# Kernel optimization log

Hardware: AMD Instinct MI355X
Metric: run time of the kernel (lower is better)

The kernel has to match this reference:

```python
import jax, jax.numpy as jnp
import numpy as np

DIM = 2048
NUM_HEADS = 16
HEAD_DIM = DIM // NUM_HEADS  # 128
B, L = 2, 2048


def setup_inputs() -> dict:
    key = jax.random.key(0)
    ks = jax.random.split(key, 5)
    x = jax.random.normal(ks[0], (B, L, DIM), dtype=jnp.float32)
    # genuine RoPE tables: inv_freq over half the head dim
    half = HEAD_DIM // 2
    inv_freq = 1.0 / (10000.0 ** (jnp.arange(half, dtype=jnp.float32) / half))
    ang = jnp.arange(L, dtype=jnp.float32)[:, None] * inv_freq[None, :]  # (L, half)
    cos = jnp.cos(ang)[:, None, :]  # (L, 1, half) broadcasts over (B,L,H,half)
    sin = jnp.sin(ang)[:, None, :]
    def dw_init(k, shape):
        fan_in, fan_out = shape
        std = 1.0 / np.sqrt(fan_in) * min(1.0, np.sqrt(fan_out / fan_in))
        return jax.random.normal(k, shape, dtype=jnp.float32) * std
    Wq = dw_init(ks[1], (DIM, DIM))
    Wk = dw_init(ks[2], (DIM, HEAD_DIM))
    Wv = dw_init(ks[3], (DIM, HEAD_DIM))
    Wo = dw_init(ks[4], (DIM, DIM))  # random instead of zeros so output is nontrivial
    return {"x": x, "cos": cos, "sin": sin, "Wq": Wq, "Wk": Wk, "Wv": Wv, "Wo": Wo}


def apply_rotary_emb(x, cos, sin):
    x1, x2 = jnp.split(x, 2, axis=-1)
    return jnp.concatenate([x1 * cos + x2 * sin, x1 * -sin + x2 * cos], axis=-1)


def rms_norm(x):
    return x * jax.lax.rsqrt(jnp.mean(x * x, axis=-1, keepdims=True) + 1e-6)


def reference(x, cos, sin, Wq, Wk, Wv, Wo):
    Bb, Ll, _ = x.shape
    q = (x @ Wq).reshape(Bb, Ll, NUM_HEADS, HEAD_DIM)  # (B,L,H,D)
    k = (x @ Wk)  # (B,L,D)  single KV head (MQA)
    v = (x @ Wv)  # (B,L,D)
    q = rms_norm(apply_rotary_emb(q, cos, sin))
    k = rms_norm(apply_rotary_emb(k[:, :, None, :], cos, sin))[:, :, 0, :]  # (B,L,D)
    scale = 1.0 / jnp.sqrt(jnp.asarray(HEAD_DIM, dtype=x.dtype))
    # scores without materializing broadcasted K: (B,H,Lq,Lk)
    scores = jnp.einsum('bqhd,bkd->bhqk', q, k) * scale
    causal = jnp.tril(jnp.ones((Ll, Ll), dtype=jnp.bool_))
    scores = jnp.where(causal[None, None], scores, jnp.asarray(-jnp.inf, dtype=scores.dtype))
    attn = jax.nn.softmax(scores, axis=-1)
    out = jnp.einsum('bhqk,bkd->bqhd', attn, v).reshape(Bb, Ll, DIM)
    return out @ Wo
```

## Files before the change

### kernel.cpp

```cpp
#include <hip/hip_runtime.h>

#define DIM 2048
#define NH 16
#define HD 128
#define BB 2
#define LL 2048
#define MROWS (BB * LL)
#define NKV 2304
#define NT 32

typedef __attribute__((ext_vector_type(8))) short short8;
typedef __attribute__((ext_vector_type(4))) float floatx4;

__device__ inline ushort f2bf(float f) {
    union { float f; unsigned u; } v; v.f = f;
    unsigned r = v.u + 0x7FFFu + ((v.u >> 16) & 1u);
    return (ushort)(r >> 16);
}

__device__ __forceinline__ ushort f2bf_fast(float f) {
    __bf16 h = (__bf16)f;
    return __builtin_bit_cast(unsigned short, h);
}

#define GL16(g, l)                                                         \
    __builtin_amdgcn_global_load_lds(                                      \
        (const __attribute__((address_space(1))) unsigned int*)(g),        \
        (__attribute__((address_space(3))) unsigned int*)(l), 16, 0, 0)

__device__ __forceinline__ short8 ld8(const ushort* p) {
    return *reinterpret_cast<const short8*>(p);
}

__global__ __launch_bounds__(256) void prep(const float* __restrict__ x,
                                            ushort* __restrict__ xb,
                                            const float* __restrict__ Wq,
                                            const float* __restrict__ Wk,
                                            const float* __restrict__ Wv,
                                            const float* __restrict__ Wo,
                                            ushort* __restrict__ Wcatt,
                                            ushort* __restrict__ Wot) {
    __shared__ ushort T[64][72];
    const int bid = blockIdx.x;
    const int tid = threadIdx.x;
    if (bid < 4096) {
        size_t i = ((size_t)bid * 256 + tid) * 8;
        float4 a = *reinterpret_cast<const float4*>(x + i);
        float4 b = *reinterpret_cast<const float4*>(x + i + 4);
        ushort o[8] = {f2bf(a.x), f2bf(a.y), f2bf(a.z), f2bf(a.w),
                       f2bf(b.x), f2bf(b.y), f2bf(b.z), f2bf(b.w)};
        *reinterpret_cast<uint4*>(xb + i) = *reinterpret_cast<uint4*>(o);
        return;
    }
    const int wb = bid - 4096;
    const float* in;
    ushort* out;
    int in_ld, c0, r0;
    const int out_ld = 2048;
    if (wb < 1024) {
        in = Wq; out = Wcatt; in_ld = 2048;
        c0 = (wb & 31) * 64; r0 = (wb >> 5) * 64;
    } else if (wb < 2048) {
        int t = wb - 1024;
        in = Wo; out = Wot; in_ld = 2048;
        c0 = (t & 31) * 64; r0 = (t >> 5) * 64;
    } else if (wb < 2112) {
        int t = wb - 2048;
        in = Wk; out = Wcatt + (size_t)2048 * 2048; in_ld = 128;
        c0 = (t & 1) * 64; r0 = (t >> 1) * 64;
    } else {
        int t = wb - 2112;
        in = Wv; out = Wcatt + (size_t)2176 * 2048; in_ld = 128;
        c0 = (t & 1) * 64; r0 = (t >> 1) * 64;
    }
#pragma unroll
    for (int rep = 0; rep < 4; ++rep) {
        int idx = tid + rep * 256;
        int r = idx >> 4, c4 = idx & 15;
        float4 f = *reinterpret_cast<const float4*>(
            in + (size_t)(r0 + r) * in_ld + c0 + c4 * 4);
        T[r][c4 * 4 + 0] = f2bf(f.x);
        T[r][c4 * 4 + 1] = f2bf(f.y);
        T[r][c4 * 4 + 2] = f2bf(f.z);
        T[r][c4 * 4 + 3] = f2bf(f.w);
    }
    __syncthreads();
#pragma unroll
    for (int rep = 0; rep < 4; ++rep) {
        int idx = tid + rep * 256;
        int cr = idx >> 4, rc4 = idx & 15;
        uint a0 = (uint)T[rc4 * 4 + 0][cr] | ((uint)T[rc4 * 4 + 1][cr] << 16);
        uint a1 = (uint)T[rc4 * 4 + 2][cr] | ((uint)T[rc4 * 4 + 3][cr] << 16);
        uint2 val = {a0, a1};
        *reinterpret_cast<uint2*>(
            out + (size_t)(c0 + cr) * out_ld + r0 + rc4 * 4) = val;
    }
}

template <int U>
__device__ __forceinline__ void stage_unit(const ushort* __restrict__ A,
                                           const ushort* __restrict__ Bt,
                                           ushort* lbase, uint offA, uint offB,
                                           int t) {
    if (t >= NT) return;
    const ushort* g = (U < 2) ? Bt : A;
    uint off = ((U < 2) ? offB : offA) + ((U & 1) ? 128u * 2048u : 0u) +
               (uint)t * 64u;
    ushort* l = lbase + U * 8192;
    GL16(g + off, l + (size_t)threadIdx.x * 8);
    GL16(g + off + 64u * 2048u, l + (size_t)(threadIdx.x + 512) * 8);
}

__global__ __launch_bounds__(512)
__attribute__((amdgpu_waves_per_eu(2, 2)))
void gemm2p(const ushort* __restrict__ A,
            const ushort* __restrict__ Bt,
            float* __restrict__ Y, int N) {
    __shared__ __attribute__((aligned(16))) ushort lds[65536];
    const int tid = threadIdx.x;
    const int lane = tid & 63;
    const int w = tid >> 6;
    const int wm = w >> 2, wn = w & 3;
    const int col = lane & 15, quad = lane >> 4;
    const int sel = col & 7;
    const int L = blockIdx.y * 9 + blockIdx.x;
    const int x8 = L & 7, jj = L >> 3;
    const int bx = jj % 9;
    const int by = x8 * 2 + jj / 9;
    const int m0 = by * 256, n0 = bx * 256;

    const int r0 = tid >> 3;
    const int gc0 = (tid & 7) ^ (r0 & 7);
    const uint offA = (uint)(m0 + r0) * 2048u + (uint)gc0 * 8u;
    const uint offB = (uint)(n0 + r0) * 2048u + (uint)gc0 * 8u;

    floatx4 acc[8][4];
#pragma unroll
    for (int mt = 0; mt < 8; ++mt)
#pragma unroll
        for (int nt = 0; nt < 4; ++nt) acc[mt][nt] = (floatx4){0.f, 0.f, 0.f, 0.f};

    const int aoff0 = (2 + wm) * 8192 + col * 64;
    const int boff0 = (wn >> 1) * 8192 + ((wn & 1) * 64 + col) * 64;
    const int koff0 = (quad ^ sel) * 8;
    const int koff1 = ((4 + quad) ^ sel) * 8;

    stage_unit<0>(A, Bt, lds, offA, offB, 0);
    stage_unit<1>(A, Bt, lds, offA, offB, 0);
    stage_unit<2>(A, Bt, lds, offA, offB, 0);
    stage_unit<3>(A, Bt, lds, offA, offB, 0);
    asm volatile("s_waitcnt vmcnt(0)" ::: "memory");
    __builtin_amdgcn_s_barrier();

#pragma unroll 2
    for (int t = 0; t < NT; ++t) {
        ushort* lb = lds + (t & 1) * 32768;
        ushort* lbn = lds + ((t + 1) & 1) * 32768;

        short8 a0[8], b0[4];
#pragma unroll
        for (int mt = 0; mt < 8; ++mt)
            a0[mt] = ld8(lb + aoff0 + mt * 1024 + koff0);
#pragma unroll
        for (int nt = 0; nt < 4; ++nt)
            b0[nt] = ld8(lb + boff0 + nt * 1024 + koff0);
        stage_unit<0>(A, Bt, lbn, offA, offB, t + 1);
        stage_unit<1>(A, Bt, lbn, offA, offB, t + 1);
        stage_unit<2>(A, Bt, lbn, offA, offB, t + 1);
        stage_unit<3>(A, Bt, lbn, offA, offB, t + 1);
        __builtin_amdgcn_s_setprio(1);
#pragma unroll
        for (int mt = 0; mt < 8; ++mt)
#pragma unroll
            for (int nt = 0; nt < 4; ++nt)
                acc[mt][nt] = __builtin_amdgcn_mfma_f32_16x16x32_bf16(
                    a0[mt], b0[nt], acc[mt][nt], 0, 0, 0);
        __builtin_amdgcn_s_setprio(0);

        short8 a1[8], b1[4];
#pragma unroll
        for (int mt = 0; mt < 8; ++mt)
            a1[mt] = ld8(lb + aoff0 + mt * 1024 + koff1);
#pragma unroll
        for (int nt = 0; nt < 4; ++nt)
            b1[nt] = ld8(lb + boff0 + nt * 1024 + koff1);
        __builtin_amdgcn_s_setprio(1);
#pragma unroll
        for (int mt = 0; mt < 8; ++mt)
#pragma unroll
            for (int nt = 0; nt < 4; ++nt)
                acc[mt][nt] = __builtin_amdgcn_mfma_f32_16x16x32_bf16(
                    a1[mt], b1[nt], acc[mt][nt], 0, 0, 0);
        __builtin_amdgcn_s_setprio(0);
        asm volatile("s_waitcnt vmcnt(0)" ::: "memory");
        __builtin_amdgcn_s_barrier();
    }

#pragma unroll
    for (int mt = 0; mt < 8; ++mt)
#pragma unroll
        for (int nt = 0; nt < 4; ++nt)
#pragma unroll
            for (int rr = 0; rr < 4; ++rr)
                Y[(size_t)(m0 + wm * 128 + mt * 16 + quad * 4 + rr) * N + n0 +
                  wn * 64 + nt * 16 + col] = acc[mt][nt][rr];
}

template <int U>
__device__ __forceinline__ void stage_po(const ushort* __restrict__ A,
                                         const ushort* __restrict__ Bt,
                                         ushort* lbase, uint offA, uint offB,
                                         int t) {
    if (t >= NT) return;
    const ushort* g = (U < 2) ? Bt : A;
    uint off = ((U < 2) ? offB : offA) + ((U == 1) ? 128u * 2048u : 0u) +
               (uint)t * 64u;
    ushort* l = lbase + U * 8192;
    GL16(g + off, l + (size_t)threadIdx.x * 8);
    GL16(g + off + 64u * 2048u, l + (size_t)(threadIdx.x + 512) * 8);
}

__global__ __launch_bounds__(512)
__attribute__((amdgpu_waves_per_eu(2, 2)))
void gemm2pw(const ushort* __restrict__ A,
             const ushort* __restrict__ Bt,
             float* __restrict__ Y, int N) {
    __shared__ __attribute__((aligned(16))) ushort lds[49152];
    const int tid = threadIdx.x;
    const int lane = tid & 63;
    const int w = tid >> 6;
    const int wm = w >> 2, wn = w & 3;
    const int col = lane & 15, quad = lane >> 4;
    const int sel = col & 7;
    const int L = blockIdx.y * 8 + blockIdx.x;
    const int x8 = L & 7, jj = L >> 3;
    const int bx = (x8 & 1) * 4 + (jj & 3);
    const int by = (x8 >> 1) * 8 + (jj >> 2);
    const int m0 = by * 128, n0 = bx * 256;

    const int r0 = tid >> 3;
    const int gc0 = (tid & 7) ^ (r0 & 7);
    const uint offA = (uint)(m0 + r0) * 2048u + (uint)gc0 * 8u;
    const uint offB = (uint)(n0 + r0) * 2048u + (uint)gc0 * 8u;

    floatx4 acc[4][4];
#pragma unroll
    for (int mt = 0; mt < 4; ++mt)
#pragma unroll
        for (int nt = 0; nt < 4; ++nt) acc[mt][nt] = (floatx4){0.f, 0.f, 0.f, 0.f};

    const int aoff0 = 16384 + wm * 4096 + col * 64;
    const int boff0 = (wn >> 1) * 8192 + ((wn & 1) * 64 + col) * 64;
    const int koff0 = (quad ^ sel) * 8;
    const int koff1 = ((4 + quad) ^ sel) * 8;

    stage_po<0>(A, Bt, lds, offA, offB, 0);
    stage_po<1>(A, Bt, lds, offA, offB, 0);
    stage_po<2>(A, Bt, lds, offA, offB, 0);
    asm volatile("s_waitcnt vmcnt(0)" ::: "memory");
    __builtin_amdgcn_s_barrier();

#pragma unroll 2
    for (int t = 0; t < NT; ++t) {
        ushort* lb = lds + (t & 1) * 24576;
        ushort* lbn = lds + ((t + 1) & 1) * 24576;

        short8 a0[4], b0[4];
#pragma unroll
        for (int mt = 0; mt < 4; ++mt)
            a0[mt] = ld8(lb + aoff0 + mt * 1024 + koff0);
#pragma unroll
        for (int nt = 0; nt < 4; ++nt)
            b0[nt] = ld8(lb + boff0 + nt * 1024 + koff0);
        stage_po<0>(A, Bt, lbn, offA, offB, t + 1);
        stage_po<1>(A, Bt, lbn, offA, offB, t + 1);
        stage_po<2>(A, Bt, lbn, offA, offB, t + 1);
        __builtin_amdgcn_s_setprio(1);
#pragma unroll
        for (int mt = 0; mt < 4; ++mt)
#pragma unroll
            for (int nt = 0; nt < 4; ++nt)
                acc[mt][nt] = __builtin_amdgcn_mfma_f32_16x16x32_bf16(
                    a0[mt], b0[nt], acc[mt][nt], 0, 0, 0);
        __builtin_amdgcn_s_setprio(0);

        short8 a1[4], b1[4];
#pragma unroll
        for (int mt = 0; mt < 4; ++mt)
            a1[mt] = ld8(lb + aoff0 + mt * 1024 + koff1);
#pragma unroll
        for (int nt = 0; nt < 4; ++nt)
            b1[nt] = ld8(lb + boff0 + nt * 1024 + koff1);
        __builtin_amdgcn_s_setprio(1);
#pragma unroll
        for (int mt = 0; mt < 4; ++mt)
#pragma unroll
            for (int nt = 0; nt < 4; ++nt)
                acc[mt][nt] = __builtin_amdgcn_mfma_f32_16x16x32_bf16(
                    a1[mt], b1[nt], acc[mt][nt], 0, 0, 0);
        __builtin_amdgcn_s_setprio(0);
        asm volatile("s_waitcnt vmcnt(0)" ::: "memory");
        __builtin_amdgcn_s_barrier();
    }

#pragma unroll
    for (int mt = 0; mt < 4; ++mt)
#pragma unroll
        for (int nt = 0; nt < 4; ++nt)
#pragma unroll
            for (int rr = 0; rr < 4; ++rr)
                Y[(size_t)(m0 + wm * 64 + mt * 16 + quad * 4 + rr) * N + n0 +
                  wn * 64 + nt * 16 + col] = acc[mt][nt][rr];
}

__device__ __forceinline__ void rope_row(const float* __restrict__ in,
                                         ushort* __restrict__ outb,
                                         const float* __restrict__ cosb,
                                         const float* __restrict__ sinb,
                                         int row, int heads, int in_ld,
                                         int lane) {
    int token = row / heads, head = row % heads;
    int l = token & (LL - 1);
    const float* p = in + (size_t)token * in_ld + head * HD;
    float x1 = p[lane];
    float x2 = p[lane + 64];
    float c = cosb[l * 64 + lane];
    float s = sinb[l * 64 + lane];
    float o1 = x1 * c + x2 * s;
    float o2 = -x1 * s + x2 * c;
    float ss = o1 * o1 + o2 * o2;
#pragma unroll
    for (int off = 32; off > 0; off >>= 1) ss += __shfl_xor(ss, off);
    float r = rsqrtf(ss * (1.0f / 128.0f) + 1e-6f);
    outb[(size_t)row * HD + lane] = f2bf(o1 * r);
    outb[(size_t)row * HD + lane + 64] = f2bf(o2 * r);
}

__global__ __launch_bounds__(256) void rope_vt(const float* __restrict__ qkv,
                                               ushort* __restrict__ qb,
                                               ushort* __restrict__ kb,
                                               ushort* __restrict__ vt,
                                               const float* __restrict__ cosb,
                                               const float* __restrict__ sinb) {
    __shared__ ushort T[64][72];
    const int bid = blockIdx.x;
    const int tid = threadIdx.x;
    const int lane = tid & 63;
    if (bid < 16384) {
        int row = bid * 4 + (tid >> 6);
        rope_row(qkv, qb, cosb, sinb, row, NH, NKV, lane);
        return;
    }
    if (bid < 17408) {
        int row = (bid - 16384) * 4 + (tid >> 6);
        rope_row(qkv + DIM, kb, cosb, sinb, row, 1, NKV, lane);
        return;
    }
    const int t = bid - 17408;
    const int l0 = (t & 31) * 64, d0 = ((t >> 5) & 1) * 64, b = t >> 6;
    const float* v = qkv + DIM + HD;
#pragma unroll
    for (int rep = 0; rep < 4; ++rep) {
        int idx = tid + rep * 256;
        int r = idx >> 4, c4 = idx & 15;
        float4 f = *reinterpret_cast<const float4*>(
            v + (size_t)(b * LL + l0 + r) * NKV + d0 + c4 * 4);
        T[r][c4 * 4 + 0] = f2bf(f.x);
        T[r][c4 * 4 + 1] = f2bf(f.y);
        T[r][c4 * 4 + 2] = f2bf(f.z);
        T[r][c4 * 4 + 3] = f2bf(f.w);
    }
    __syncthreads();
#pragma unroll
    for (int rep = 0; rep < 4; ++rep) {
        int idx = tid + rep * 256;
        int dr = idx >> 4, lc4 = idx & 15;
        uint a0 = (uint)T[lc4 * 4 + 0][dr] | ((uint)T[lc4 * 4 + 1][dr] << 16);
        uint a1 = (uint)T[lc4 * 4 + 2][dr] | ((uint)T[lc4 * 4 + 3][dr] << 16);
        uint2 val = {a0, a1};
        *reinterpret_cast<uint2*>(
            vt + (size_t)(b * HD + d0 + dr) * LL + l0 + lc4 * 4) = val;
    }
}

__global__ __launch_bounds__(256) void flash_mfma(const ushort* __restrict__ qb,
                                                  const ushort* __restrict__ kb,
                                                  const ushort* __restrict__ vt,
                                                  ushort* __restrict__ aob) {
    __shared__ ushort Ks[64 * 128];
    __shared__ ushort VTs[128 * 64];
    __shared__ ushort Ps[4][16][68];

    const int tid = threadIdx.x;
    const int w = tid >> 6, lane = tid & 63;
    const int col = lane & 15, quad = lane >> 4;
    const int pairIdx = blockIdx.x, bh = blockIdx.y;
    const int b = bh >> 4, h = bh & 15;
    const int sel = col & 7;
    const float scl2 = 0.08838834764831845f * 1.44269504088896340736f;
    const float M2 = 11.5f * 1.44269504088896340736f;

    const int ksr[4] = {(tid + 0) >> 4, (tid + 256) >> 4, (tid + 512) >> 4,
                        (tid + 768) >> 4};
    const int vsr[4] = {(tid + 0) >> 3, (tid + 256) >> 3, (tid + 512) >> 3,
                        (tid + 768) >> 3};

    for (int sp = 0; sp < 2; ++sp) {
        const int qt = sp ? (31 - pairIdx) : pairIdx;
        const int q0 = qt * 64;

        const ushort* qrow =
            qb + ((size_t)(b * LL + q0 + w * 16 + col) * NH + h) * HD;
        short8 aq[4];
#pragma unroll
        for (int kc = 0; kc < 4; ++kc)
            aq[kc] = *reinterpret_cast<const short8*>(qrow + kc * 32 + quad * 8);

        float lrow[4] = {0.f, 0.f, 0.f, 0.f};
        floatx4 oacc[8];
#pragma unroll
        for (int dt = 0; dt < 8; ++dt) oacc[dt] = (floatx4){0.f, 0.f, 0.f, 0.f};

        const int ntiles = qt + 1;
        for (int kt = 0; kt < ntiles; ++kt) {
            const int k0 = kt * 64;
            __syncthreads();
#pragma unroll
            for (int rep = 0; rep < 4; ++rep) {
                int slot = tid + rep * 256;
                int r = ksr[rep];
                int gc = (slot & 15) ^ (r & 7);
                GL16(kb + (size_t)(b * LL + k0 + r) * HD + gc * 8,
                     Ks + (size_t)slot * 8);
            }
#pragma unroll
            for (int rep = 0; rep < 4; ++rep) {
                int slot = tid + rep * 256;
                int r = vsr[rep];
                int gc = (slot & 7) ^ (r & 7);
                GL16(vt + (size_t)(b * HD + r) * LL + k0 + gc * 8,
                     VTs + (size_t)slot * 8);
            }
            __syncthreads();

            floatx4 sacc[4];
#pragma unroll
            for (int nt = 0; nt < 4; ++nt)
                sacc[nt] = (floatx4){0.f, 0.f, 0.f, 0.f};
            __builtin_amdgcn_s_setprio(1);
#pragma unroll
            for (int nt = 0; nt < 4; ++nt) {
#pragma unroll
                for (int kc = 0; kc < 4; ++kc) {
                    short8 bk = *reinterpret_cast<const short8*>(
                        &Ks[(nt * 16 + col) * 128 +
                            ((kc * 4 + quad) ^ sel) * 8]);
                    sacc[nt] = __builtin_amdgcn_mfma_f32_16x16x32_bf16(
                        aq[kc], bk, sacc[nt], 0, 0, 0);
                }
            }
            __builtin_amdgcn_s_setprio(0);

            float psum[4] = {0.f, 0.f, 0.f, 0.f};
            if (kt == qt) {
#pragma unroll
                for (int nt = 0; nt < 4; ++nt) {
                    int kj = k0 + nt * 16 + col;
#pragma unroll
                    for (int rr = 0; rr < 4; ++rr) {
                        int qi = q0 + w * 16 + quad * 4 + rr;
                        float p = exp2f(fmaf(sacc[nt][rr], scl2, -M2));
                        p = (kj <= qi) ? p : 0.0f;
                        sacc[nt][rr] = p;
                        psum[rr] += p;
                    }
                }
            } else {
#pragma unroll
                for (int nt = 0; nt < 4; ++nt)
#pragma unroll
                    for (int rr = 0; rr < 4; ++rr) {
                        float p = exp2f(fmaf(sacc[nt][rr], scl2, -M2));
                        sacc[nt][rr] = p;
                        psum[rr] += p;
                    }
            }
#pragma unroll
            for (int rr = 0; rr < 4; ++rr) lrow[rr] += psum[rr];

#pragma unroll
            for (int nt = 0; nt < 4; ++nt)
#pragma unroll
                for (int rr = 0; rr < 4; ++rr)
                    Ps[w][quad * 4 + rr][nt * 16 + col] =
                        f2bf_fast(sacc[nt][rr]);
            asm volatile("s_waitcnt lgkmcnt(0)" ::: "memory");

#pragma unroll
            for (int kt2 = 0; kt2 < 2; ++kt2) {
                short8 ap = *reinterpret_cast<const short8*>(
                    &Ps[w][col][kt2 * 32 + quad * 8]);
                __builtin_amdgcn_s_setprio(1);
#pragma unroll
                for (int dt = 0; dt < 8; ++dt) {
                    short8 bv = *reinterpret_cast<const short8*>(
                        &VTs[(dt * 16 + col) * 64 +
                             ((kt2 * 4 + quad) ^ sel) * 8]);
                    oacc[dt] = __builtin_amdgcn_mfma_f32_16x16x32_bf16(
                        ap, bv, oacc[dt], 0, 0, 0);
                }
                __builtin_amdgcn_s_setprio(0);
            }
        }

#pragma unroll
        for (int off = 1; off < 16; off <<= 1)
#pragma unroll
            for (int rr = 0; rr < 4; ++rr)
                lrow[rr] += __shfl_xor(lrow[rr], off);
        float inv[4];
#pragma unroll
        for (int rr = 0; rr < 4; ++rr) inv[rr] = 1.0f / lrow[rr];
#pragma unroll
        for (int dt = 0; dt < 8; ++dt)
#pragma unroll
            for (int rr = 0; rr < 4; ++rr)
                aob[((size_t)(b * LL + q0 + w * 16 + quad * 4 + rr) * NH + h) *
                        HD + dt * 16 + col] =
                    f2bf_fast(oacc[dt][rr] * inv[rr]);
    }
}

extern "C" void kernel_launch(void* const* d_in, const int* in_sizes, int n_in,
                              void* d_out, int out_size, void* d_ws,
                              size_t ws_size, hipStream_t stream) {
    const float* x    = (const float*)d_in[0];
    const float* cosb = (const float*)d_in[1];
    const float* sinb = (const float*)d_in[2];
    const float* Wq   = (const float*)d_in[3];
    const float* Wk   = (const float*)d_in[4];
    const float* Wv   = (const float*)d_in[5];
    const float* Wo   = (const float*)d_in[6];
    float* out = (float*)d_out;

    float* qkv  = (float*)d_ws;
    ushort* xb  = (ushort*)(qkv + (size_t)MROWS * NKV);
    ushort* qb  = xb + (size_t)MROWS * DIM;
    ushort* kb  = qb + (size_t)MROWS * DIM;
    ushort* vt  = kb + (size_t)MROWS * HD;
    ushort* aob = vt + (size_t)MROWS * HD;
    ushort* Wcatt = aob + (size_t)MROWS * DIM;
    ushort* Wot   = Wcatt + (size_t)NKV * DIM;

    prep<<<dim3(4096 + 2176), 256, 0, stream>>>(x, xb, Wq, Wk, Wv, Wo, Wcatt,
                                                Wot);

    gemm2p<<<dim3(NKV / 256, MROWS / 256), 512, 0, stream>>>(xb, Wcatt, qkv,
                                                             NKV);

    rope_vt<<<dim3(16384 + 1024 + 128), 256, 0, stream>>>(qkv, qb, kb, vt,
                                                          cosb, sinb);

    flash_mfma<<<dim3(LL / 128, BB * NH), 256, 0, stream>>>(qb, kb, vt, aob);

    gemm2pw<<<dim3(DIM / 256, MROWS / 128), 512, 0, stream>>>(aob, Wot, out,
                                                              DIM);
}
```

Measured before the change: 277.4 us.

## Shrink QKV projection GEMM tile to 128x128 with 256-thread blocks

Replaces the 256x256-tile, 512-thread QKV GEMM with a 128x128-tile, 256-thread variant, remapping the block swizzle and LDS staging to match. This raises the grid from 144 to 576 blocks so that all compute units are occupied on this problem shape. In exchange, each block gets less operand reuse and global/L2 traffic per FLOP rises.

```diff
diff --git a/kernel.cpp b/kernel.cpp
--- a/kernel.cpp
+++ b/kernel.cpp
@@ -97,96 +97,88 @@
     }
 }
 
-template <int U>
-__device__ __forceinline__ void stage_unit(const ushort* __restrict__ A,
-                                           const ushort* __restrict__ Bt,
-                                           ushort* lbase, uint offA, uint offB,
-                                           int t) {
-    if (t >= NT) return;
-    const ushort* g = (U < 2) ? Bt : A;
-    uint off = ((U < 2) ? offB : offA) + ((U & 1) ? 128u * 2048u : 0u) +
-               (uint)t * 64u;
-    ushort* l = lbase + U * 8192;
-    GL16(g + off, l + (size_t)threadIdx.x * 8);
-    GL16(g + off + 64u * 2048u, l + (size_t)(threadIdx.x + 512) * 8);
-}
-
-__global__ __launch_bounds__(512)
+__global__ __launch_bounds__(256)
 __attribute__((amdgpu_waves_per_eu(2, 2)))
-void gemm2p(const ushort* __restrict__ A,
-            const ushort* __restrict__ Bt,
-            float* __restrict__ Y, int N) {
-    __shared__ __attribute__((aligned(16))) ushort lds[65536];
+void gemm2p128(const ushort* __restrict__ A,
+               const ushort* __restrict__ Bt,
+               float* __restrict__ Y, int N) {
+    __shared__ __attribute__((aligned(16))) ushort lds[32768];
     const int tid = threadIdx.x;
     const int lane = tid & 63;
     const int w = tid >> 6;
-    const int wm = w >> 2, wn = w & 3;
+    const int wm = w >> 1, wn = w & 1;
     const int col = lane & 15, quad = lane >> 4;
     const int sel = col & 7;
-    const int L = blockIdx.y * 9 + blockIdx.x;
+    const int L = blockIdx.y * 18 + blockIdx.x;
     const int x8 = L & 7, jj = L >> 3;
-    const int bx = jj % 9;
-    const int by = x8 * 2 + jj / 9;
-    const int m0 = by * 256, n0 = bx * 256;
+    const int bx = (x8 & 1) * 9 + jj % 9;
+    const int by = (x8 >> 1) * 8 + jj / 9;
+    const int m0 = by * 128, n0 = bx * 128;
 
     const int r0 = tid >> 3;
     const int gc0 = (tid & 7) ^ (r0 & 7);
     const uint offA = (uint)(m0 + r0) * 2048u + (uint)gc0 * 8u;
     const uint offB = (uint)(n0 + r0) * 2048u + (uint)gc0 * 8u;
 
-    floatx4 acc[8][4];
-#pragma unroll
-    for (int mt = 0; mt < 8; ++mt)
+    floatx4 acc[4][4];
+#pragma unroll
+    for (int mt = 0; mt < 4; ++mt)
 #pragma unroll
         for (int nt = 0; nt < 4; ++nt) acc[mt][nt] = (floatx4){0.f, 0.f, 0.f, 0.f};
 
-    const int aoff0 = (2 + wm) * 8192 + col * 64;
-    const int boff0 = (wn >> 1) * 8192 + ((wn & 1) * 64 + col) * 64;
+    const int aoff0 = wm * 4096 + col * 64;
+    const int boff0 = 8192 + wn * 4096 + col * 64;
     const int koff0 = (quad ^ sel) * 8;
     const int koff1 = ((4 + quad) ^ sel) * 8;
 
-    stage_unit<0>(A, Bt, lds, offA, offB, 0);
-    stage_unit<1>(A, Bt, lds, offA, offB, 0);
-    stage_unit<2>(A, Bt, lds, offA, offB, 0);
-    stage_unit<3>(A, Bt, lds, offA, offB, 0);
+    auto stage = [&](ushort* lbase, int t) {
+        if (t >= NT) return;
+        uint tk = (uint)t * 64u;
+#pragma unroll
+        for (int rep = 0; rep < 4; ++rep) {
+            GL16(A + offA + rep * 65536u + tk,
+                 lbase + (size_t)(tid + rep * 256) * 8);
+            GL16(Bt + offB + rep * 65536u + tk,
+                 lbase + 8192 + (size_t)(tid + rep * 256) * 8);
+        }
+    };
+
+    stage(lds, 0);
     asm volatile("s_waitcnt vmcnt(0)" ::: "memory");
     __builtin_amdgcn_s_barrier();
 
 #pragma unroll 2
     for (int t = 0; t < NT; ++t) {
-        ushort* lb = lds + (t & 1) * 32768;
-        ushort* lbn = lds + ((t + 1) & 1) * 32768;
-
-        short8 a0[8], b0[4];
-#pragma unroll
-        for (int mt = 0; mt < 8; ++mt)
+        ushort* lb = lds + (t & 1) * 16384;
+        ushort* lbn = lds + ((t + 1) & 1) * 16384;
+
+        short8 a0[4], b0[4];
+#pragma unroll
+        for (int mt = 0; mt < 4; ++mt)
             a0[mt] = ld8(lb + aoff0 + mt * 1024 + koff0);
 #pragma unroll
         for (int nt = 0; nt < 4; ++nt)
             b0[nt] = ld8(lb + boff0 + nt * 1024 + koff0);
-        stage_unit<0>(A, Bt, lbn, offA, offB, t + 1);
-        stage_unit<1>(A, Bt, lbn, offA, offB, t + 1);
-        stage_unit<2>(A, Bt, lbn, offA, offB, t + 1);
-        stage_unit<3>(A, Bt, lbn, offA, offB, t + 1);
+        stage(lbn, t + 1);
         __builtin_amdgcn_s_setprio(1);
 #pragma unroll
-        for (int mt = 0; mt < 8; ++mt)
+        for (int mt = 0; mt < 4; ++mt)
 #pragma unroll
             for (int nt = 0; nt < 4; ++nt)
                 acc[mt][nt] = __builtin_amdgcn_mfma_f32_16x16x32_bf16(
                     a0[mt], b0[nt], acc[mt][nt], 0, 0, 0);
         __builtin_amdgcn_s_setprio(0);
 
-        short8 a1[8], b1[4];
-#pragma unroll
-        for (int mt = 0; mt < 8; ++mt)
+        short8 a1[4], b1[4];
+#pragma unroll
+        for (int mt = 0; mt < 4; ++mt)
             a1[mt] = ld8(lb + aoff0 + mt * 1024 + koff1);
 #pragma unroll
         for (int nt = 0; nt < 4; ++nt)
             b1[nt] = ld8(lb + boff0 + nt * 1024 + koff1);
         __builtin_amdgcn_s_setprio(1);
 #pragma unroll
-        for (int mt = 0; mt < 8; ++mt)
+        for (int mt = 0; mt < 4; ++mt)
 #pragma unroll
             for (int nt = 0; nt < 4; ++nt)
                 acc[mt][nt] = __builtin_amdgcn_mfma_f32_16x16x32_bf16(
@@ -197,12 +189,12 @@
     }
 
 #pragma unroll
-    for (int mt = 0; mt < 8; ++mt)
+    for (int mt = 0; mt < 4; ++mt)
 #pragma unroll
         for (int nt = 0; nt < 4; ++nt)
 #pragma unroll
             for (int rr = 0; rr < 4; ++rr)
-                Y[(size_t)(m0 + wm * 128 + mt * 16 + quad * 4 + rr) * N + n0 +
+                Y[(size_t)(m0 + wm * 64 + mt * 16 + quad * 4 + rr) * N + n0 +
                   wn * 64 + nt * 16 + col] = acc[mt][nt][rr];
 }
 
@@ -555,8 +547,8 @@
     prep<<<dim3(4096 + 2176), 256, 0, stream>>>(x, xb, Wq, Wk, Wv, Wo, Wcatt,
                                                 Wot);
 
-    gemm2p<<<dim3(NKV / 256, MROWS / 256), 512, 0, stream>>>(xb, Wcatt, qkv,
-                                                             NKV);
+    gemm2p128<<<dim3(NKV / 128, MROWS / 128), 256, 0, stream>>>(xb, Wcatt,
+                                                                qkv, NKV);
 
     rope_vt<<<dim3(16384 + 1024 + 128), 256, 0, stream>>>(qkv, qb, kb, vt,
                                                           cosb, sinb);
```

Result: slower. 292.5 us (+5.4%).
